# Performance work log

Measured on AMD Instinct MI355X. Metric: run time of the kernel, lower is better.

The kernel has to match this reference:

```python
import jax, jax.numpy as jnp
import numpy as np

D_MODEL = 2048
D_COMPARE = 2048
D_MEMORY = 2048
N_HEADS = 16
KV_HEADS = 4
KV_REPEAT = N_HEADS // KV_HEADS          # 4
C_HD = D_COMPARE // N_HEADS              # 128 compare head dim
M_HD = D_MEMORY // N_HEADS               # 128 memory head dim
TOTAL_OUT = D_COMPARE + KV_HEADS * C_HD + KV_HEADS * M_HD  # 3072


def setup_inputs() -> dict:
    key = jax.random.key(0)
    ks = jax.random.split(key, 5)
    b, t = 2, 2048
    x = jax.random.normal(ks[0], (b, t, D_MODEL), dtype=jnp.float32)
    s_in = 1.0 / np.sqrt(D_MODEL)
    s_out = 1.0 / np.sqrt(D_MEMORY)
    in_w = jax.random.uniform(ks[1], (TOTAL_OUT, D_MODEL), jnp.float32, -s_in, s_in)
    in_b = jax.random.uniform(ks[2], (TOTAL_OUT,), jnp.float32, -s_in, s_in)
    out_w = jax.random.uniform(ks[3], (D_MODEL, D_MEMORY), jnp.float32, -s_out, s_out)
    out_b = jax.random.uniform(ks[4], (D_MODEL,), jnp.float32, -s_out, s_out)
    return {"x": x, "in_w": in_w, "in_b": in_b, "out_w": out_w, "out_b": out_b}


def reference(x, in_w, in_b, out_w, out_b):
    b, t, _ = x.shape
    packed = jnp.einsum("btd,od->bto", x, in_w) + in_b          # [b,t,TOTAL_OUT]
    q, k, v = jnp.split(packed, [D_COMPARE, D_COMPARE + KV_HEADS * C_HD], axis=-1)
    # q: [b, kv, rep, t, hd] -- head h maps to kv group h // KV_REPEAT
    # (torch repeat_interleave on KV head dim == grouped reshape of q heads)
    q = q.reshape(b, t, KV_HEADS, KV_REPEAT, C_HD).transpose(0, 2, 3, 1, 4)
    k = k.reshape(b, t, KV_HEADS, C_HD).transpose(0, 2, 1, 3)   # [b,kv,t,hd]
    v = v.reshape(b, t, KV_HEADS, M_HD).transpose(0, 2, 1, 3)   # [b,kv,t,mhd]
    scale = 1.0 / np.sqrt(C_HD)
    scores = jnp.einsum("bgrqd,bgkd->bgrqk", q, k) * scale      # [b,kv,rep,t,t]
    attn = jax.nn.softmax(scores, axis=-1)
    y = jnp.einsum("bgrqk,bgkd->bgrqd", attn, v)                # [b,kv,rep,t,mhd]
    y = y.transpose(0, 3, 1, 2, 4).reshape(b, t, D_MEMORY)      # heads back in order
    return jnp.einsum("btm,dm->btd", y, out_w) + out_b
```

## Files before the change

kernel.cpp:

```cpp
#include <hip/hip_runtime.h>
#include <hip/hip_bf16.h>
#include <stdint.h>

#define DEV __device__ __forceinline__

typedef __attribute__((ext_vector_type(8))) short bf16x8;
typedef __attribute__((ext_vector_type(4))) float f32x4;

DEV unsigned short f2bf(float f) {
  unsigned u = __builtin_bit_cast(unsigned, f);
  unsigned r = u + 0x7FFF + ((u >> 16) & 1);
  return (unsigned short)(r >> 16);
}

DEV unsigned short f2bfh(float f) {
  __bf16 h = (__bf16)f;
  return __builtin_bit_cast(unsigned short, h);
}

typedef __attribute__((address_space(1))) void gvoid;
typedef __attribute__((address_space(3))) void lvoid;

DEV void g2l16(const void* g, void* l) {
  __builtin_amdgcn_global_load_lds((gvoid*)g, (lvoid*)l, 16, 0, 0);
}

#define MFMA16(a, b, c) __builtin_amdgcn_mfma_f32_16x16x32_bf16(a, b, c, 0, 0, 0)

__global__ void k_cvt3(const float* __restrict__ x, unsigned short* __restrict__ xo, int nx4,
                       const float* __restrict__ w, unsigned short* __restrict__ wo, int nw4,
                       const float* __restrict__ v, unsigned short* __restrict__ vo, int nv4) {
  int i = blockIdx.x * blockDim.x + threadIdx.x;
  int stride = gridDim.x * blockDim.x;
  int tot = nx4 + nw4 + nv4;
  for (; i < tot; i += stride) {
    const float* src; unsigned short* dst; int j = i;
    if (j < nx4) { src = x; dst = xo; }
    else if ((j -= nx4) < nw4) { src = w; dst = wo; }
    else { j -= nw4; src = v; dst = vo; }
    float4 val = reinterpret_cast<const float4*>(src)[j];
    ushort4 o;
    o.x = f2bf(val.x); o.y = f2bf(val.y); o.z = f2bf(val.z); o.w = f2bf(val.w);
    reinterpret_cast<ushort4*>(dst)[j] = o;
  }
}

template<bool BF16OUT>
__global__ __launch_bounds__(256, 2) void k_gemm(
    const unsigned short* __restrict__ A, const unsigned short* __restrict__ B,
    const float* __restrict__ bias, void* __restrict__ C,
    int M, int N, int K) {
  __shared__ unsigned short As[128 * 32];
  __shared__ unsigned short Bs[128 * 32];
  int tid = threadIdx.x;
  int lane = tid & 63, wid = tid >> 6;
  int bm = blockIdx.y * 128, bn = blockIdx.x * 128;
  int wm = (wid >> 1) * 64, wn = (wid & 1) * 64;
  int row16 = lane & 15, kq = lane >> 4;
  f32x4 acc[4][4] = {};
  int r = tid >> 2, c = (tid & 3) * 8;
  const unsigned short* Ag = A + (size_t)(bm + r) * K + c;
  const unsigned short* Bg = B + (size_t)(bn + r) * K + c;
  for (int k0 = 0; k0 < K; k0 += 32) {
    g2l16(Ag + k0, &As[tid * 8]);
    g2l16(Ag + (size_t)64 * K + k0, &As[2048 + tid * 8]);
    g2l16(Bg + k0, &Bs[tid * 8]);
    g2l16(Bg + (size_t)64 * K + k0, &Bs[2048 + tid * 8]);
    __syncthreads();
    bf16x8 a[4], b[4];
#pragma unroll
    for (int m = 0; m < 4; m++) a[m] = *(const bf16x8*)&As[(wm + m * 16 + row16) * 32 + kq * 8];
#pragma unroll
    for (int n = 0; n < 4; n++) b[n] = *(const bf16x8*)&Bs[(wn + n * 16 + row16) * 32 + kq * 8];
    __builtin_amdgcn_s_setprio(1);
#pragma unroll
    for (int m = 0; m < 4; m++)
#pragma unroll
      for (int n = 0; n < 4; n++)
        acc[m][n] = MFMA16(a[m], b[n], acc[m][n]);
    __builtin_amdgcn_s_setprio(0);
    __syncthreads();
  }
#pragma unroll
  for (int n = 0; n < 4; n++) {
    int col = bn + wn + n * 16 + row16;
    float bv = bias[col];
#pragma unroll
    for (int m = 0; m < 4; m++) {
      int rw = bm + wm + m * 16 + kq * 4;
#pragma unroll
      for (int j = 0; j < 4; j++) {
        float v = acc[m][n][j] + bv;
        if (BF16OUT) ((unsigned short*)C)[(size_t)(rw + j) * N + col] = f2bf(v);
        else         ((float*)C)[(size_t)(rw + j) * N + col] = v;
      }
    }
  }
}

__global__ void k_vt(const unsigned short* __restrict__ packed, unsigned short* __restrict__ vT) {
  __shared__ unsigned short tile[64][136];
  int g = blockIdx.y;
  int b = g >> 2, kv = g & 3;
  int t0 = blockIdx.x * 64;
  int tid = threadIdx.x;
#pragma unroll
  for (int i = 0; i < 4; i++) {
    int tl = i * 16 + (tid >> 4);
    int d0 = (tid & 15) * 8;
    bf16x8 v = *(const bf16x8*)&packed[(size_t)(b * 2048 + t0 + tl) * 3072 + 2560 + kv * 128 + d0];
    *(bf16x8*)&tile[tl][d0] = v;
  }
  __syncthreads();
  int d = tid >> 1, ts = (tid & 1) * 32;
  size_t obase = (size_t)(g * 128 + d) * 2048 + t0 + ts;
#pragma unroll
  for (int j = 0; j < 4; j++) {
    bf16x8 o;
#pragma unroll
    for (int e = 0; e < 8; e++) o[e] = (short)tile[ts + j * 8 + e][d];
    *(bf16x8*)&vT[obase + j * 8] = o;
  }
}

__global__ __launch_bounds__(256, 2) void k_flash(
    const unsigned short* __restrict__ packed,
    const unsigned short* __restrict__ vT,
    unsigned short* __restrict__ Y) {
  __shared__ unsigned short Ks[2][64 * 128];
  __shared__ unsigned short Vs[128 * 64];
  __shared__ unsigned short Ps[4][2][16 * 68];
  __shared__ float Axc[4][2][16];
  int tid = threadIdx.x, lane = tid & 63, wid = tid >> 6;
  int row16 = lane & 15, kq = lane >> 4;
  int r3 = row16 & 7;
  int g = blockIdx.x;
  int s8 = g & 7;
  int b = s8 >> 2, kv = s8 & 3;
  int w = g >> 3;
  int h = kv * 4 + (w & 3);
  int qt = w >> 2;
  size_t prow = (size_t)b * 2048;

  unsigned short* Q = &Ks[0][0];
  {
    int rr = tid >> 4;
    int cc = ((tid & 15) ^ (rr & 7)) * 8;
    const unsigned short* qg = packed + (prow + qt * 128 + rr) * 3072 + h * 128 + cc;
#pragma unroll
    for (int i = 0; i < 8; i++)
      g2l16(qg + (size_t)i * 16 * 3072, &Q[i * 2048 + tid * 8]);
  }
  asm volatile("s_waitcnt vmcnt(0)" ::: "memory");
  __builtin_amdgcn_s_barrier();
  bf16x8 q[2][4];
#pragma unroll
  for (int qi = 0; qi < 2; qi++)
#pragma unroll
    for (int kc = 0; kc < 4; kc++)
      q[qi][kc] = *(const bf16x8*)&Q[(qi * 64 + wid * 16 + row16) * 128 + (((kc * 4 + kq) ^ r3) * 8)];
  asm volatile("s_waitcnt lgkmcnt(0)" ::: "memory");
  __builtin_amdgcn_sched_barrier(0);
  __builtin_amdgcn_s_barrier();

  const unsigned short* kg0 = packed + prow * 3072 + 2048 + kv * 128;
  const unsigned short* vg0 = vT + (size_t)(b * 4 + kv) * 128 * 2048;
  int krr = tid >> 4;
  int kcc = ((tid & 15) ^ (krr & 7)) * 8;
  int vrr = tid >> 3;
  int vcc = ((tid & 7) ^ (vrr & 7)) * 8;

  auto stageK = [&](int t, int kbuf) {
    const unsigned short* kg = kg0 + (size_t)(t * 64 + krr) * 3072 + kcc;
#pragma unroll
    for (int i = 0; i < 4; i++)
      g2l16(kg + (size_t)i * 16 * 3072, &Ks[kbuf][i * 2048 + tid * 8]);
  };
  auto stageV = [&](int t) {
    const unsigned short* vg = vg0 + (size_t)vrr * 2048 + t * 64 + vcc;
#pragma unroll
    for (int i = 0; i < 4; i++)
      g2l16(vg + (size_t)i * 32 * 2048, &Vs[i * 2048 + tid * 8]);
  };

  stageK(0, 0);
  stageV(0);
  asm volatile("s_waitcnt vmcnt(4)" ::: "memory");
  __builtin_amdgcn_s_barrier();

  f32x4 o[2][8] = {};
  float mr[2] = {-1e30f, -1e30f}, lr[2] = {0.f, 0.f};
  const float sc2 = 0.08838834764831845f * 1.4426950408889634f;

  for (int t = 0; t < 32; t++) {
    int kb = t & 1;
    int tn = t < 31 ? t + 1 : 31;

    f32x4 st[2][4];
#pragma unroll
    for (int qi = 0; qi < 2; qi++)
#pragma unroll
      for (int mk = 0; mk < 4; mk++) st[qi][mk] = f32x4{0.f, 0.f, 0.f, 0.f};
#pragma unroll
    for (int mk = 0; mk < 4; mk++) {
      bf16x8 bk[4];
#pragma unroll
      for (int kc = 0; kc < 4; kc++)
        bk[kc] = *(const bf16x8*)&Ks[kb][(mk * 16 + row16) * 128 + (((kc * 4 + kq) ^ r3) * 8)];
      __builtin_amdgcn_s_setprio(1);
#pragma unroll
      for (int kc = 0; kc < 4; kc++) {
        st[0][mk] = MFMA16(bk[kc], q[0][kc], st[0][mk]);
        st[1][mk] = MFMA16(bk[kc], q[1][kc], st[1][mk]);
      }
      __builtin_amdgcn_s_setprio(0);
    }

    stageK(tn, kb ^ 1);

    float pmax[2];
#pragma unroll
    for (int qi = 0; qi < 2; qi++) {
      float a0 = fmaxf(fmaxf(st[qi][0][0], st[qi][0][1]), fmaxf(st[qi][0][2], st[qi][0][3]));
      float a1 = fmaxf(fmaxf(st[qi][1][0], st[qi][1][1]), fmaxf(st[qi][1][2], st[qi][1][3]));
      float a2 = fmaxf(fmaxf(st[qi][2][0], st[qi][2][1]), fmaxf(st[qi][2][2], st[qi][2][3]));
      float a3 = fmaxf(fmaxf(st[qi][3][0], st[qi][3][1]), fmaxf(st[qi][3][2], st[qi][3][3]));
      float p = fmaxf(fmaxf(a0, a1), fmaxf(a2, a3));
      p = fmaxf(p, __shfl_xor(p, 16));
      p = fmaxf(p, __shfl_xor(p, 32));
      pmax[qi] = p * sc2;
    }
    if (!__all(pmax[0] <= mr[0] + 8.f && pmax[1] <= mr[1] + 8.f)) {
#pragma unroll
      for (int qi = 0; qi < 2; qi++) {
        float mn = fmaxf(mr[qi], pmax[qi]);
        float al = exp2f(mr[qi] - mn);
        mr[qi] = mn;
        lr[qi] *= al;
        if (lane < 16) Axc[wid][qi][row16] = al;
      }
#pragma unroll
      for (int qi = 0; qi < 2; qi++) {
        float alo[4];
#pragma unroll
        for (int j = 0; j < 4; j++) alo[j] = Axc[wid][qi][kq * 4 + j];
#pragma unroll
        for (int np = 0; np < 8; np++)
#pragma unroll
          for (int j = 0; j < 4; j++) o[qi][np][j] *= alo[j];
      }
    }
#pragma unroll
    for (int qi = 0; qi < 2; qi++) {
      float nm = -mr[qi];
#pragma unroll
      for (int mk = 0; mk < 4; mk++)
#pragma unroll
        for (int j = 0; j < 4; j++)
          st[qi][mk][j] = exp2f(fmaf(st[qi][mk][j], sc2, nm));
      float s0 = (st[qi][0][0] + st[qi][0][1]) + (st[qi][0][2] + st[qi][0][3]);
      float s1 = (st[qi][1][0] + st[qi][1][1]) + (st[qi][1][2] + st[qi][1][3]);
      float s2 = (st[qi][2][0] + st[qi][2][1]) + (st[qi][2][2] + st[qi][2][3]);
      float s3 = (st[qi][3][0] + st[qi][3][1]) + (st[qi][3][2] + st[qi][3][3]);
      float rs = (s0 + s1) + (s2 + s3);
      rs += __shfl_xor(rs, 16);
      rs += __shfl_xor(rs, 32);
      lr[qi] += rs;
    }

    bf16x8 pf[2][2];
#pragma unroll
    for (int qi = 0; qi < 2; qi++) {
#pragma unroll
      for (int mk = 0; mk < 4; mk++) {
        ushort4 pw;
        pw.x = f2bfh(st[qi][mk][0]); pw.y = f2bfh(st[qi][mk][1]);
        pw.z = f2bfh(st[qi][mk][2]); pw.w = f2bfh(st[qi][mk][3]);
        *(ushort4*)&Ps[wid][qi][row16 * 68 + mk * 16 + kq * 4] = pw;
      }
#pragma unroll
      for (int k2 = 0; k2 < 2; k2++)
        pf[qi][k2] = *(const bf16x8*)&Ps[wid][qi][row16 * 68 + k2 * 32 + kq * 8];
    }

    asm volatile("s_waitcnt vmcnt(4)" ::: "memory");
    __builtin_amdgcn_s_barrier();

#pragma unroll
    for (int np = 0; np < 8; np++) {
      int vrow = np * 16 + row16;
      bf16x8 bv0 = *(const bf16x8*)&Vs[vrow * 64 + ((kq ^ r3) * 8)];
      bf16x8 bv1 = *(const bf16x8*)&Vs[vrow * 64 + (((4 + kq) ^ r3) * 8)];
      __builtin_amdgcn_s_setprio(1);
      o[0][np] = MFMA16(pf[0][0], bv0, o[0][np]);
      o[0][np] = MFMA16(pf[0][1], bv1, o[0][np]);
      o[1][np] = MFMA16(pf[1][0], bv0, o[1][np]);
      o[1][np] = MFMA16(pf[1][1], bv1, o[1][np]);
      __builtin_amdgcn_s_setprio(0);
    }

    __builtin_amdgcn_s_barrier();
    stageV(tn);
    asm volatile("s_waitcnt vmcnt(4)" ::: "memory");
    __builtin_amdgcn_s_barrier();
  }
  asm volatile("s_waitcnt vmcnt(0)" ::: "memory");

#pragma unroll
  for (int qi = 0; qi < 2; qi++)
    if (lane < 16) Axc[wid][qi][row16] = lr[qi];
#pragma unroll
  for (int qi = 0; qi < 2; qi++)
#pragma unroll
    for (int j = 0; j < 4; j++) {
      float inv = 1.f / Axc[wid][qi][kq * 4 + j];
      size_t orow = prow + (size_t)qt * 128 + qi * 64 + wid * 16 + kq * 4 + j;
#pragma unroll
      for (int np = 0; np < 8; np++)
        Y[orow * 2048 + h * 128 + np * 16 + row16] = f2bfh(o[qi][np][j] * inv);
    }
}

extern "C" void kernel_launch(void* const* d_in, const int* in_sizes, int n_in,
                              void* d_out, int out_size, void* d_ws, size_t ws_size,
                              hipStream_t stream) {
  const float* x     = (const float*)d_in[0];
  const float* in_w  = (const float*)d_in[1];
  const float* in_b  = (const float*)d_in[2];
  const float* out_w = (const float*)d_in[3];
  const float* out_b = (const float*)d_in[4];
  float* out = (float*)d_out;

  unsigned short* xb     = (unsigned short*)d_ws;
  unsigned short* wb     = xb + 8388608;
  unsigned short* owb    = wb + 6291456;
  unsigned short* packed = owb + 4194304;
  unsigned short* vt     = packed + 12582912;
  unsigned short* y      = vt + 2097152;

  k_cvt3<<<dim3(2048), dim3(256), 0, stream>>>(x, xb, 8388608 / 4,
                                               in_w, wb, 6291456 / 4,
                                               out_w, owb, 4194304 / 4);

  k_gemm<true><<<dim3(24, 32), dim3(256), 0, stream>>>(xb, wb, in_b, packed, 4096, 3072, 2048);
  k_vt<<<dim3(32, 8), dim3(256), 0, stream>>>(packed, vt);
  k_flash<<<dim3(512), dim3(256), 0, stream>>>(packed, vt, y);
  k_gemm<false><<<dim3(16, 32), dim3(256), 0, stream>>>(y, owb, out_b, out, 4096, 2048, 2048);
}
```

Before: 230.0 us.

## Use 8 waves per flash block with one 16-row Q tile each; MFMA row sums

The flash-attention block grows from 4 to 8 waves, and each wave now owns a single 16-row query slice instead of two. This halves per-wave register state and raises occupancy, and the K/V staging loads are split across twice as many threads. The softmax row-sum shuffles are replaced by extra MFMAs against a vector of ones that accumulate alongside O. In exchange, each wave reuses every LDS-loaded K/V fragment less, which raises LDS read traffic per FLOP, and block barriers now synchronize more waves.

```diff
diff --git a/kernel.cpp b/kernel.cpp
--- a/kernel.cpp
+++ b/kernel.cpp
@@ -123,14 +123,14 @@
   }
 }
 
-__global__ __launch_bounds__(256, 2) void k_flash(
+__global__ __launch_bounds__(512, 4) void k_flash(
     const unsigned short* __restrict__ packed,
     const unsigned short* __restrict__ vT,
     unsigned short* __restrict__ Y) {
   __shared__ unsigned short Ks[2][64 * 128];
   __shared__ unsigned short Vs[128 * 64];
-  __shared__ unsigned short Ps[4][2][16 * 68];
-  __shared__ float Axc[4][2][16];
+  __shared__ unsigned short Ps[8][16 * 72];
+  __shared__ float Axc[8][16];
   int tid = threadIdx.x, lane = tid & 63, wid = tid >> 6;
   int row16 = lane & 15, kq = lane >> 4;
   int r3 = row16 & 7;
@@ -148,17 +148,15 @@
     int cc = ((tid & 15) ^ (rr & 7)) * 8;
     const unsigned short* qg = packed + (prow + qt * 128 + rr) * 3072 + h * 128 + cc;
 #pragma unroll
-    for (int i = 0; i < 8; i++)
-      g2l16(qg + (size_t)i * 16 * 3072, &Q[i * 2048 + tid * 8]);
+    for (int i = 0; i < 4; i++)
+      g2l16(qg + (size_t)i * 32 * 3072, &Q[i * 4096 + tid * 8]);
   }
   asm volatile("s_waitcnt vmcnt(0)" ::: "memory");
   __builtin_amdgcn_s_barrier();
-  bf16x8 q[2][4];
-#pragma unroll
-  for (int qi = 0; qi < 2; qi++)
-#pragma unroll
-    for (int kc = 0; kc < 4; kc++)
-      q[qi][kc] = *(const bf16x8*)&Q[(qi * 64 + wid * 16 + row16) * 128 + (((kc * 4 + kq) ^ r3) * 8)];
+  bf16x8 q[4];
+#pragma unroll
+  for (int kc = 0; kc < 4; kc++)
+    q[kc] = *(const bf16x8*)&Q[(wid * 16 + row16) * 128 + (((kc * 4 + kq) ^ r3) * 8)];
   asm volatile("s_waitcnt lgkmcnt(0)" ::: "memory");
   __builtin_amdgcn_sched_barrier(0);
   __builtin_amdgcn_s_barrier();
@@ -173,117 +171,93 @@
   auto stageK = [&](int t, int kbuf) {
     const unsigned short* kg = kg0 + (size_t)(t * 64 + krr) * 3072 + kcc;
 #pragma unroll
-    for (int i = 0; i < 4; i++)
-      g2l16(kg + (size_t)i * 16 * 3072, &Ks[kbuf][i * 2048 + tid * 8]);
+    for (int i = 0; i < 2; i++)
+      g2l16(kg + (size_t)i * 32 * 3072, &Ks[kbuf][i * 4096 + tid * 8]);
   };
   auto stageV = [&](int t) {
     const unsigned short* vg = vg0 + (size_t)vrr * 2048 + t * 64 + vcc;
 #pragma unroll
-    for (int i = 0; i < 4; i++)
-      g2l16(vg + (size_t)i * 32 * 2048, &Vs[i * 2048 + tid * 8]);
+    for (int i = 0; i < 2; i++)
+      g2l16(vg + (size_t)i * 64 * 2048, &Vs[i * 4096 + tid * 8]);
   };
 
   stageK(0, 0);
   stageV(0);
-  asm volatile("s_waitcnt vmcnt(4)" ::: "memory");
+  asm volatile("s_waitcnt vmcnt(2)" ::: "memory");
   __builtin_amdgcn_s_barrier();
 
-  f32x4 o[2][8] = {};
-  float mr[2] = {-1e30f, -1e30f}, lr[2] = {0.f, 0.f};
+  f32x4 o[8] = {};
+  f32x4 ls = {};
+  float mr = -1e30f;
   const float sc2 = 0.08838834764831845f * 1.4426950408889634f;
+  bf16x8 ones;
+#pragma unroll
+  for (int e = 0; e < 8; e++) ones[e] = (short)0x3F80;
 
   for (int t = 0; t < 32; t++) {
     int kb = t & 1;
     int tn = t < 31 ? t + 1 : 31;
 
-    f32x4 st[2][4];
-#pragma unroll
-    for (int qi = 0; qi < 2; qi++)
-#pragma unroll
-      for (int mk = 0; mk < 4; mk++) st[qi][mk] = f32x4{0.f, 0.f, 0.f, 0.f};
+    f32x4 st[4];
 #pragma unroll
     for (int mk = 0; mk < 4; mk++) {
+      st[mk] = f32x4{0.f, 0.f, 0.f, 0.f};
       bf16x8 bk[4];
 #pragma unroll
       for (int kc = 0; kc < 4; kc++)
         bk[kc] = *(const bf16x8*)&Ks[kb][(mk * 16 + row16) * 128 + (((kc * 4 + kq) ^ r3) * 8)];
       __builtin_amdgcn_s_setprio(1);
 #pragma unroll
-      for (int kc = 0; kc < 4; kc++) {
-        st[0][mk] = MFMA16(bk[kc], q[0][kc], st[0][mk]);
-        st[1][mk] = MFMA16(bk[kc], q[1][kc], st[1][mk]);
-      }
+      for (int kc = 0; kc < 4; kc++)
+        st[mk] = MFMA16(bk[kc], q[kc], st[mk]);
       __builtin_amdgcn_s_setprio(0);
     }
 
     stageK(tn, kb ^ 1);
 
-    float pmax[2];
-#pragma unroll
-    for (int qi = 0; qi < 2; qi++) {
-      float a0 = fmaxf(fmaxf(st[qi][0][0], st[qi][0][1]), fmaxf(st[qi][0][2], st[qi][0][3]));
-      float a1 = fmaxf(fmaxf(st[qi][1][0], st[qi][1][1]), fmaxf(st[qi][1][2], st[qi][1][3]));
-      float a2 = fmaxf(fmaxf(st[qi][2][0], st[qi][2][1]), fmaxf(st[qi][2][2], st[qi][2][3]));
-      float a3 = fmaxf(fmaxf(st[qi][3][0], st[qi][3][1]), fmaxf(st[qi][3][2], st[qi][3][3]));
-      float p = fmaxf(fmaxf(a0, a1), fmaxf(a2, a3));
-      p = fmaxf(p, __shfl_xor(p, 16));
-      p = fmaxf(p, __shfl_xor(p, 32));
-      pmax[qi] = p * sc2;
-    }
-    if (!__all(pmax[0] <= mr[0] + 8.f && pmax[1] <= mr[1] + 8.f)) {
-#pragma unroll
-      for (int qi = 0; qi < 2; qi++) {
-        float mn = fmaxf(mr[qi], pmax[qi]);
-        float al = exp2f(mr[qi] - mn);
-        mr[qi] = mn;
-        lr[qi] *= al;
-        if (lane < 16) Axc[wid][qi][row16] = al;
-      }
-#pragma unroll
-      for (int qi = 0; qi < 2; qi++) {
-        float alo[4];
-#pragma unroll
-        for (int j = 0; j < 4; j++) alo[j] = Axc[wid][qi][kq * 4 + j];
-#pragma unroll
-        for (int np = 0; np < 8; np++)
-#pragma unroll
-          for (int j = 0; j < 4; j++) o[qi][np][j] *= alo[j];
-      }
-    }
-#pragma unroll
-    for (int qi = 0; qi < 2; qi++) {
-      float nm = -mr[qi];
-#pragma unroll
-      for (int mk = 0; mk < 4; mk++)
-#pragma unroll
-        for (int j = 0; j < 4; j++)
-          st[qi][mk][j] = exp2f(fmaf(st[qi][mk][j], sc2, nm));
-      float s0 = (st[qi][0][0] + st[qi][0][1]) + (st[qi][0][2] + st[qi][0][3]);
-      float s1 = (st[qi][1][0] + st[qi][1][1]) + (st[qi][1][2] + st[qi][1][3]);
-      float s2 = (st[qi][2][0] + st[qi][2][1]) + (st[qi][2][2] + st[qi][2][3]);
-      float s3 = (st[qi][3][0] + st[qi][3][1]) + (st[qi][3][2] + st[qi][3][3]);
-      float rs = (s0 + s1) + (s2 + s3);
-      rs += __shfl_xor(rs, 16);
-      rs += __shfl_xor(rs, 32);
-      lr[qi] += rs;
-    }
-
-    bf16x8 pf[2][2];
-#pragma unroll
-    for (int qi = 0; qi < 2; qi++) {
-#pragma unroll
-      for (int mk = 0; mk < 4; mk++) {
-        ushort4 pw;
-        pw.x = f2bfh(st[qi][mk][0]); pw.y = f2bfh(st[qi][mk][1]);
-        pw.z = f2bfh(st[qi][mk][2]); pw.w = f2bfh(st[qi][mk][3]);
-        *(ushort4*)&Ps[wid][qi][row16 * 68 + mk * 16 + kq * 4] = pw;
-      }
-#pragma unroll
-      for (int k2 = 0; k2 < 2; k2++)
-        pf[qi][k2] = *(const bf16x8*)&Ps[wid][qi][row16 * 68 + k2 * 32 + kq * 8];
-    }
-
-    asm volatile("s_waitcnt vmcnt(4)" ::: "memory");
+    float a0 = fmaxf(fmaxf(st[0][0], st[0][1]), fmaxf(st[0][2], st[0][3]));
+    float a1 = fmaxf(fmaxf(st[1][0], st[1][1]), fmaxf(st[1][2], st[1][3]));
+    float a2 = fmaxf(fmaxf(st[2][0], st[2][1]), fmaxf(st[2][2], st[2][3]));
+    float a3 = fmaxf(fmaxf(st[3][0], st[3][1]), fmaxf(st[3][2], st[3][3]));
+    float p = fmaxf(fmaxf(a0, a1), fmaxf(a2, a3));
+    p = fmaxf(p, __shfl_xor(p, 16));
+    p = fmaxf(p, __shfl_xor(p, 32));
+    p *= sc2;
+    if (!__all(p <= mr + 8.f)) {
+      float mn = fmaxf(mr, p);
+      float al = exp2f(mr - mn);
+      mr = mn;
+      if (lane < 16) Axc[wid][row16] = al;
+      float alo[4];
+#pragma unroll
+      for (int j = 0; j < 4; j++) alo[j] = Axc[wid][kq * 4 + j];
+#pragma unroll
+      for (int np = 0; np < 8; np++)
+#pragma unroll
+        for (int j = 0; j < 4; j++) o[np][j] *= alo[j];
+#pragma unroll
+      for (int j = 0; j < 4; j++) ls[j] *= alo[j];
+    }
+    float nm = -mr;
+#pragma unroll
+    for (int mk = 0; mk < 4; mk++)
+#pragma unroll
+      for (int j = 0; j < 4; j++)
+        st[mk][j] = exp2f(fmaf(st[mk][j], sc2, nm));
+
+#pragma unroll
+    for (int mk = 0; mk < 4; mk++) {
+      ushort4 pw;
+      pw.x = f2bfh(st[mk][0]); pw.y = f2bfh(st[mk][1]);
+      pw.z = f2bfh(st[mk][2]); pw.w = f2bfh(st[mk][3]);
+      *(ushort4*)&Ps[wid][row16 * 72 + mk * 16 + kq * 4] = pw;
+    }
+    bf16x8 pf[2];
+#pragma unroll
+    for (int k2 = 0; k2 < 2; k2++)
+      pf[k2] = *(const bf16x8*)&Ps[wid][row16 * 72 + k2 * 32 + kq * 8];
+
+    asm volatile("s_waitcnt vmcnt(2)" ::: "memory");
     __builtin_amdgcn_s_barrier();
 
 #pragma unroll
@@ -292,33 +266,28 @@
       bf16x8 bv0 = *(const bf16x8*)&Vs[vrow * 64 + ((kq ^ r3) * 8)];
       bf16x8 bv1 = *(const bf16x8*)&Vs[vrow * 64 + (((4 + kq) ^ r3) * 8)];
       __builtin_amdgcn_s_setprio(1);
-      o[0][np] = MFMA16(pf[0][0], bv0, o[0][np]);
-      o[0][np] = MFMA16(pf[0][1], bv1, o[0][np]);
-      o[1][np] = MFMA16(pf[1][0], bv0, o[1][np]);
-      o[1][np] = MFMA16(pf[1][1], bv1, o[1][np]);
+      o[np] = MFMA16(pf[0], bv0, o[np]);
+      o[np] = MFMA16(pf[1], bv1, o[np]);
       __builtin_amdgcn_s_setprio(0);
     }
+    ls = MFMA16(pf[0], ones, ls);
+    ls = MFMA16(pf[1], ones, ls);
 
     __builtin_amdgcn_s_barrier();
     stageV(tn);
-    asm volatile("s_waitcnt vmcnt(4)" ::: "memory");
+    asm volatile("s_waitcnt vmcnt(2)" ::: "memory");
     __builtin_amdgcn_s_barrier();
   }
   asm volatile("s_waitcnt vmcnt(0)" ::: "memory");
 
 #pragma unroll
-  for (int qi = 0; qi < 2; qi++)
-    if (lane < 16) Axc[wid][qi][row16] = lr[qi];
-#pragma unroll
-  for (int qi = 0; qi < 2; qi++)
-#pragma unroll
-    for (int j = 0; j < 4; j++) {
-      float inv = 1.f / Axc[wid][qi][kq * 4 + j];
-      size_t orow = prow + (size_t)qt * 128 + qi * 64 + wid * 16 + kq * 4 + j;
-#pragma unroll
-      for (int np = 0; np < 8; np++)
-        Y[orow * 2048 + h * 128 + np * 16 + row16] = f2bfh(o[qi][np][j] * inv);
-    }
+  for (int j = 0; j < 4; j++) {
+    float inv = 1.f / ls[j];
+    size_t orow = prow + (size_t)qt * 128 + wid * 16 + kq * 4 + j;
+#pragma unroll
+    for (int np = 0; np < 8; np++)
+      Y[orow * 2048 + h * 128 + np * 16 + row16] = f2bfh(o[np][j] * inv);
+  }
 }
 
 extern "C" void kernel_launch(void* const* d_in, const int* in_sizes, int n_in,
@@ -344,6 +313,6 @@
 
   k_gemm<true><<<dim3(24, 32), dim3(256), 0, stream>>>(xb, wb, in_b, packed, 4096, 3072, 2048);
   k_vt<<<dim3(32, 8), dim3(256), 0, stream>>>(packed, vt);
-  k_flash<<<dim3(512), dim3(256), 0, stream>>>(packed, vt, y);
+  k_flash<<<dim3(512), dim3(512), 0, stream>>>(packed, vt, y);
   k_gemm<false><<<dim3(16, 32), dim3(256), 0, stream>>>(y, owb, out_b, out, 4096, 2048, 2048);
 }
```

Result: no change. 226.3 us (-1.6%).
